# Kernel tuning notes

Measured on AMD Instinct MI355X. Metric: run time of the kernel, lower is better.

## Reference

```python
import jax, jax.numpy as jnp
import numpy as np

MASK_PENALTY = 1e15  # matches the TF module's additive mask constant


def setup_inputs() -> dict:
    key = jax.random.key(0)
    k1, k2, k3, k4, k5 = jax.random.split(key, 5)
    B, S, E, DK, DV = 4, 2048, 1024, 128, 128
    inputs = jax.random.normal(k1, (B, S, E), dtype=jnp.float32)
    mask = jax.random.randint(k2, (B, S, S), 0, 2, dtype=jnp.int32)
    # Dense kernels (glorot-ish scale)
    Wq = jax.random.normal(k3, (E, DK), dtype=jnp.float32) / np.float32(np.sqrt(E))
    Wk = jax.random.normal(k4, (E, DK), dtype=jnp.float32) / np.float32(np.sqrt(E))
    Wv = jax.random.normal(k5, (E, DV), dtype=jnp.float32) / np.float32(np.sqrt(E))
    return {"inputs": inputs, "mask": mask, "Wq": Wq, "Wk": Wk, "Wv": Wv}


def reference(inputs, mask, Wq, Wk, Wv):
    # q, k, v projections (no bias)
    q = jnp.einsum("bse,ed->bsd", inputs, Wq)  # [B,S,DK]
    k = jnp.einsum("bse,ed->bsd", inputs, Wk)  # [B,S,DK]
    v = jnp.einsum("bse,ed->bsd", inputs, Wv)  # [B,S,DV]
    dim_k = Wq.shape[-1]
    scale = jnp.asarray(1.0 / np.sqrt(dim_k), dtype=q.dtype)
    dot_p = jnp.einsum("bqd,bkd->bqk", q, k) * scale  # [B,S,S]
    dot_p = dot_p - MASK_PENALTY * mask.astype(dot_p.dtype)
    softm = jax.nn.softmax(dot_p, axis=-1)
    return jnp.einsum("bqk,bkd->bqd", softm, v)  # [B,S,DV]
```

## Files before the change

### kernel.cpp

```cpp
#include <hip/hip_runtime.h>
#include <stdint.h>


#define SEQ   2048
#define EDIM  1024
#define DDIM  128
#define QSCALE 0.08838834764831845f

typedef unsigned short u16;
using short8 = __attribute__((ext_vector_type(8))) short;
using f32x4  = __attribute__((ext_vector_type(4))) float;

__device__ __forceinline__ u16 f2bf(float x) {
    uint32_t u = __float_as_uint(x);
    return (u16)((u + 0x7fffu + ((u >> 16) & 1u)) >> 16);
}

__device__ __forceinline__ void gld16(const void* gsrc, void* lds_dst) {
    __builtin_amdgcn_global_load_lds(
        (const __attribute__((address_space(1))) uint32_t*)(uintptr_t)gsrc,
        (__attribute__((address_space(3))) uint32_t*)(uint32_t)(uintptr_t)lds_dst,
        16, 0, 0);
}

__global__ __launch_bounds__(256) void wprep_kernel(
    const float* __restrict__ Wq, const float* __restrict__ Wk, const float* __restrict__ Wv,
    u16* __restrict__ Wt)
{
    __shared__ u16 tl[64][65];
    const int t = blockIdx.x;
    const int wsel = t >> 5;
    const int tile = t & 31;
    const int k0 = (tile >> 1) * 64;
    const int n0 = (tile & 1) * 64;
    const float* W = (wsel == 0) ? Wq : ((wsel == 1) ? Wk : Wv);
#pragma unroll
    for (int it = 0; it < 16; ++it) {
        const int idx = it * 256 + threadIdx.x;
        const int r = idx >> 6, c = idx & 63;
        tl[c][r] = f2bf(W[(size_t)(k0 + r) * DDIM + n0 + c]);
    }
    __syncthreads();
    u16* Wtp = Wt + (size_t)wsel * DDIM * EDIM;
#pragma unroll
    for (int it = 0; it < 16; ++it) {
        const int idx = it * 256 + threadIdx.x;
        const int r = idx >> 6, c = idx & 63;
        Wtp[(size_t)(n0 + r) * EDIM + k0 + c] = tl[r][c];
    }
}

__global__ __launch_bounds__(256, 2) void proj_kernel(
    const float* __restrict__ Ain, const u16* __restrict__ Wtb,
    u16* __restrict__ Qb, u16* __restrict__ Kb, u16* __restrict__ Vtb)
{
    __shared__ __align__(16) uint8_t smem[24576];
    const int tid = threadIdx.x;
    const int w = tid >> 6, lane = tid & 63;
    const int lq = lane & 15, lg = lane >> 4;
    const int m0 = blockIdx.x * 64;
    const int wm = blockIdx.y;
    const u16* Wt = Wtb + (size_t)wm * DDIM * EDIM;

    f32x4 acc[8] = {};

#pragma unroll 1
    for (int kt = 0; kt < 16; ++kt) {
        const int k0 = kt * 64;
#pragma unroll
        for (int i = 0; i < 4; ++i) {
            const int G = i * 256 + tid;
            const int n = G >> 3, c = G & 7;
            gld16(Wt + (size_t)n * EDIM + k0 + (size_t)((c ^ (n & 7)) * 8),
                  smem + 8192 + i * 4096 + w * 1024);
        }
#pragma unroll
        for (int i = 0; i < 2; ++i) {
            const int G = i * 256 + tid;
            const int row = G >> 3, c = G & 7;
            const float* s2 = Ain + (size_t)(m0 + row) * EDIM + k0 + (c ^ (row & 7)) * 8;
            const f32x4 a0 = *(const f32x4*)s2;
            const f32x4 a1 = *(const f32x4*)(s2 + 4);
            short8 v;
            v[0] = (short)f2bf(a0[0]); v[1] = (short)f2bf(a0[1]);
            v[2] = (short)f2bf(a0[2]); v[3] = (short)f2bf(a0[3]);
            v[4] = (short)f2bf(a1[0]); v[5] = (short)f2bf(a1[1]);
            v[6] = (short)f2bf(a1[2]); v[7] = (short)f2bf(a1[3]);
            *(short8*)(smem + row * 128 + (c << 4)) = v;
        }
        __syncthreads();
#pragma unroll
        for (int ks = 0; ks < 2; ++ks) {
            const int arow = w * 16 + lq;
            const short8 af = *(const short8*)(smem + arow * 128 + ((((ks << 2) + lg) ^ (arow & 7)) << 4));
#pragma unroll
            for (int nf = 0; nf < 8; ++nf) {
                const int nrow = nf * 16 + lq;
                const short8 bfv = *(const short8*)(smem + 8192 + nrow * 128 + ((((ks << 2) + lg) ^ (nrow & 7)) << 4));
                acc[nf] = __builtin_amdgcn_mfma_f32_16x16x32_bf16(af, bfv, acc[nf], 0, 0, 0);
            }
        }
        __syncthreads();
    }

    if (wm < 2) {
        u16* Ot = (u16*)smem;
#pragma unroll
        for (int nf = 0; nf < 8; ++nf)
#pragma unroll
            for (int r = 0; r < 4; ++r)
                Ot[(size_t)(w * 16 + lg * 4 + r) * 128 + nf * 16 + lq] = f2bf(acc[nf][r]);
        __syncthreads();
        u16* dst = (wm == 0 ? Qb : Kb) + (size_t)m0 * 128;
#pragma unroll
        for (int i = 0; i < 4; ++i) {
            const int idx = (i * 256 + tid) * 8;
            *(short8*)(dst + idx) = *(const short8*)((const u16*)smem + idx);
        }
    } else {
#pragma unroll
        for (int nf = 0; nf < 8; ++nf)
#pragma unroll
            for (int r = 0; r < 4; ++r) {
                const int srow = w * 16 + lg * 4 + r;
                const int dcol = nf * 16 + lq;
                *(u16*)(smem + dcol * 128 + (((srow >> 3) ^ (dcol & 7)) << 4) + (srow & 7) * 2) = f2bf(acc[nf][r]);
            }
        __syncthreads();
        const int b = m0 >> 11;
        const int s0b = m0 & 2047;
        u16* dst = Vtb + (size_t)b * DDIM * SEQ;
#pragma unroll
        for (int i = 0; i < 4; ++i) {
            const int idx = i * 256 + tid;
            const int dd = idx >> 3, c = idx & 7;
            const short8 v2 = *(const short8*)(smem + dd * 128 + ((c ^ (dd & 7)) << 4));
            *(short8*)(dst + (size_t)dd * SEQ + s0b + c * 8) = v2;
        }
    }
}

__global__ __launch_bounds__(256, 2) void flash_kernel(
    const int* __restrict__ mask,
    const u16* __restrict__ Qb, const u16* __restrict__ Kb, const u16* __restrict__ Vtb,
    float* __restrict__ out)
{
    __shared__ __align__(16) uint8_t smem[69632];
    __shared__ float ml_m[4][16], ml_l[4][16], recipL[16];

    const int tid = threadIdx.x;
    const int w = tid >> 6, lane = tid & 63;
    const int lq = lane & 15, lg = lane >> 4;

    const int qt = blockIdx.x;
    const int b = qt >> 7;
    const int q0 = (qt & 127) << 4;
    const size_t qrow0 = (size_t)b * SEQ + q0;

    const u16* Qp = Qb + qrow0 * 128;
    const u16* Kp = Kb + (size_t)b * SEQ * 128;
    const u16* Vp = Vtb + (size_t)b * DDIM * SEQ;
    const int* mp = mask + ((size_t)b * SEQ + q0) * SEQ;

    short8 qf[4];
#pragma unroll
    for (int ks = 0; ks < 4; ++ks)
        qf[ks] = *(const short8*)(Qp + (size_t)lq * 128 + ks * 32 + lg * 8);

    f32x4 acc[8] = {};
    float mrow[4], lrow[4];
#pragma unroll
    for (int r = 0; r < 4; ++r) { mrow[r] = -1e30f; lrow[r] = 0.0f; }

    uint8_t* kvbase = smem + w * 16384;

#pragma unroll 1
    for (int t = 0; t < 16; ++t) {
        const int kv0 = w * 512 + t * 32;
        asm volatile("s_waitcnt lgkmcnt(0)" ::: "memory");
#pragma unroll
        for (int i = 0; i < 8; ++i) {
            const int G = i * 64 + lane;
            const int row = G >> 4, c = G & 15;
            gld16(Kp + (size_t)(kv0 + row) * 128 + (c ^ (row & 7)) * 8,
                  kvbase + i * 1024);
        }
#pragma unroll
        for (int i = 0; i < 8; ++i) {
            const int G = i * 64 + lane;
            const int dd = G >> 2, c = G & 3;
            gld16(Vp + (size_t)dd * SEQ + kv0 + (c ^ ((dd ^ (dd >> 2)) & 3)) * 8,
                  kvbase + 8192 + i * 1024);
        }
        int mv[2][4];
#pragma unroll
        for (int nf = 0; nf < 2; ++nf)
#pragma unroll
            for (int r = 0; r < 4; ++r)
                mv[nf][r] = mp[(size_t)(lg * 4 + r) * SEQ + kv0 + nf * 16 + lq];

        asm volatile("s_waitcnt vmcnt(0)" ::: "memory");

        f32x4 sacc[2] = {};
#pragma unroll
        for (int ks = 0; ks < 4; ++ks) {
#pragma unroll
            for (int nf = 0; nf < 2; ++nf) {
                const int krow = nf * 16 + lq;
                const short8 kf = *(const short8*)(kvbase + krow * 256 + ((((ks << 2) + lg) ^ (krow & 7)) << 4));
                sacc[nf] = __builtin_amdgcn_mfma_f32_16x16x32_bf16(qf[ks], kf, sacc[nf], 0, 0, 0);
            }
        }

        float sv[2][4], tm[4];
#pragma unroll
        for (int nf = 0; nf < 2; ++nf)
#pragma unroll
            for (int r = 0; r < 4; ++r)
                sv[nf][r] = sacc[nf][r] * QSCALE - 1e15f * (float)mv[nf][r];
#pragma unroll
        for (int r = 0; r < 4; ++r) tm[r] = fmaxf(sv[0][r], sv[1][r]);
#pragma unroll
        for (int d = 1; d < 16; d <<= 1)
#pragma unroll
            for (int r = 0; r < 4; ++r)
                tm[r] = fmaxf(tm[r], __shfl_xor(tm[r], d));

        float sf[4];
#pragma unroll
        for (int r = 0; r < 4; ++r) {
            const float mnew = fmaxf(mrow[r], tm[r]);
            sf[r] = __expf(mrow[r] - mnew);
            mrow[r] = mnew;
        }
        float p[2][4], rs[4];
#pragma unroll
        for (int nf = 0; nf < 2; ++nf)
#pragma unroll
            for (int r = 0; r < 4; ++r)
                p[nf][r] = __expf(sv[nf][r] - mrow[r]);
#pragma unroll
        for (int r = 0; r < 4; ++r) rs[r] = p[0][r] + p[1][r];
#pragma unroll
        for (int d = 1; d < 16; d <<= 1)
#pragma unroll
            for (int r = 0; r < 4; ++r)
                rs[r] += __shfl_xor(rs[r], d);
#pragma unroll
        for (int r = 0; r < 4; ++r) lrow[r] = lrow[r] * sf[r] + rs[r];
#pragma unroll
        for (int df = 0; df < 8; ++df)
#pragma unroll
            for (int r = 0; r < 4; ++r)
                acc[df][r] *= sf[r];

        uint8_t* pbase = smem + 65536 + w * 1024;
#pragma unroll
        for (int nf = 0; nf < 2; ++nf)
#pragma unroll
            for (int r = 0; r < 4; ++r) {
                const int row = lg * 4 + r, col = nf * 16 + lq;
                *(u16*)(pbase + row * 64 + ((((col >> 3) ^ ((row ^ (row >> 2)) & 3))) << 4) + (col & 7) * 2)
                    = f2bf(p[nf][r]);
            }
        const short8 pf = *(const short8*)(pbase + lq * 64 + ((lg ^ ((lq ^ (lq >> 2)) & 3)) << 4));
#pragma unroll
        for (int nf = 0; nf < 8; ++nf) {
            const int dd = nf * 16 + lq;
            const short8 vf = *(const short8*)(kvbase + 8192 + dd * 64 + ((lg ^ ((dd ^ (dd >> 2)) & 3)) << 4));
            acc[nf] = __builtin_amdgcn_mfma_f32_16x16x32_bf16(pf, vf, acc[nf], 0, 0, 0);
        }
    }

    if (lq == 0) {
#pragma unroll
        for (int r = 0; r < 4; ++r) {
            ml_m[w][lg * 4 + r] = mrow[r];
            ml_l[w][lg * 4 + r] = lrow[r];
        }
    }
    __syncthreads();
    float Lg[4];
#pragma unroll
    for (int r = 0; r < 4; ++r) {
        const int row = lg * 4 + r;
        const float m0v = ml_m[0][row], m1v = ml_m[1][row], m2v = ml_m[2][row], m3v = ml_m[3][row];
        const float mm = fmaxf(fmaxf(m0v, m1v), fmaxf(m2v, m3v));
        Lg[r] = ml_l[0][row] * __expf(m0v - mm) + ml_l[1][row] * __expf(m1v - mm)
              + ml_l[2][row] * __expf(m2v - mm) + ml_l[3][row] * __expf(m3v - mm);
        const float s = __expf(mrow[r] - mm);
#pragma unroll
        for (int df = 0; df < 8; ++df) acc[df][r] *= s;
    }
    if (w == 0 && lq == 0) {
#pragma unroll
        for (int r = 0; r < 4; ++r) recipL[lg * 4 + r] = 1.0f / Lg[r];
    }
    float* Ol = (float*)smem;
#pragma unroll
    for (int df = 0; df < 8; ++df)
#pragma unroll
        for (int r = 0; r < 4; ++r)
            Ol[(size_t)(w * 16 + lg * 4 + r) * 128 + df * 16 + lq] = acc[df][r];
    __syncthreads();

    {
        const int idx = tid * 8;
        const int row = idx >> 7, c0 = idx & 127;
        const float rl = recipL[row];
        f32x4 s0 = {}, s1 = {};
#pragma unroll
        for (int wv = 0; wv < 4; ++wv) {
            const float* p2 = Ol + (size_t)(wv * 16 + row) * 128 + c0;
            s0 += *(const f32x4*)p2;
            s1 += *(const f32x4*)(p2 + 4);
        }
        s0 *= rl; s1 *= rl;
        float* op = out + (qrow0 + row) * 128 + c0;
        *(f32x4*)op = s0;
        *(f32x4*)(op + 4) = s1;
    }
}

extern "C" void kernel_launch(void* const* d_in, const int* in_sizes, int n_in,
                              void* d_out, int out_size, void* d_ws, size_t ws_size,
                              hipStream_t stream) {
    (void)in_sizes; (void)n_in; (void)out_size; (void)ws_size;
    const float* inputs = (const float*)d_in[0];
    const int*   mask   = (const int*)d_in[1];
    const float* Wq     = (const float*)d_in[2];
    const float* Wk     = (const float*)d_in[3];
    const float* Wv     = (const float*)d_in[4];
    float* out = (float*)d_out;

    uint8_t* ws = (uint8_t*)d_ws;
    u16* Wtb = (u16*)ws;
    u16* Qb  = (u16*)(ws + 786432);
    u16* Kb  = (u16*)(ws + 2883584);
    u16* Vtb = (u16*)(ws + 4980736);

    hipLaunchKernelGGL(wprep_kernel, dim3(96), dim3(256), 0, stream, Wq, Wk, Wv, Wtb);
    hipLaunchKernelGGL(proj_kernel, dim3(128, 3), dim3(256), 0, stream, inputs, Wtb, Qb, Kb, Vtb);
    hipLaunchKernelGGL(flash_kernel, dim3(512), dim3(256), 0, stream, mask, Qb, Kb, Vtb, out);
}
```

Before: 184.4 us.

## Bit-pack mask in prep pass, retile projection GEMM, fold Q scale, split waits

The int32 mask is packed into 32-bit bitmasks by a combined prep kernel, so the attention kernel reads 1 bit per mask element instead of 4 bytes. The projection GEMM moves to 128x128 tiles with a 2x2 wave layout and an XCD-aware block remap. The softmax scale is folded into Q at projection time. The flash kernel now waits only on K loads before QK^T and defers the V wait until the PV step. The flash blocks are also remapped across XCDs. The mask is still read in full once in prep, and the bigger projection tiles cut the grid to 192 blocks, which lowers parallelism.

Measured after the change: 188.4 us. 2.2% more time.

```diff
diff --git a/kernel.cpp b/kernel.cpp
--- a/kernel.cpp
+++ b/kernel.cpp
@@ -8,8 +8,10 @@
 #define QSCALE 0.08838834764831845f
 
 typedef unsigned short u16;
+typedef unsigned int   u32;
 using short8 = __attribute__((ext_vector_type(8))) short;
 using f32x4  = __attribute__((ext_vector_type(4))) float;
+using int4v  = __attribute__((ext_vector_type(4))) int;
 
 __device__ __forceinline__ u16 f2bf(float x) {
     uint32_t u = __float_as_uint(x);
@@ -23,30 +25,47 @@
         16, 0, 0);
 }
 
-__global__ __launch_bounds__(256) void wprep_kernel(
+__global__ __launch_bounds__(256) void prep_kernel(
+    const int* __restrict__ mask,
     const float* __restrict__ Wq, const float* __restrict__ Wk, const float* __restrict__ Wv,
-    u16* __restrict__ Wt)
+    u32* __restrict__ Mbits, u16* __restrict__ Wt)
 {
     __shared__ u16 tl[64][65];
-    const int t = blockIdx.x;
-    const int wsel = t >> 5;
-    const int tile = t & 31;
-    const int k0 = (tile >> 1) * 64;
-    const int n0 = (tile & 1) * 64;
-    const float* W = (wsel == 0) ? Wq : ((wsel == 1) ? Wk : Wv);
-#pragma unroll
-    for (int it = 0; it < 16; ++it) {
-        const int idx = it * 256 + threadIdx.x;
-        const int r = idx >> 6, c = idx & 63;
-        tl[c][r] = f2bf(W[(size_t)(k0 + r) * DDIM + n0 + c]);
-    }
-    __syncthreads();
-    u16* Wtp = Wt + (size_t)wsel * DDIM * EDIM;
-#pragma unroll
-    for (int it = 0; it < 16; ++it) {
-        const int idx = it * 256 + threadIdx.x;
-        const int r = idx >> 6, c = idx & 63;
-        Wtp[(size_t)(n0 + r) * EDIM + k0 + c] = tl[r][c];
+    const int bx = blockIdx.x;
+    if (bx < 2048) {
+        const int word = bx * 256 + threadIdx.x;
+        const int* src = mask + (size_t)word * 32;
+        u32 bits = 0;
+#pragma unroll
+        for (int it = 0; it < 8; ++it) {
+            const int4v v = *(const int4v*)(src + it * 4);
+            bits |= (v[0] != 0 ? 1u : 0u) << (it * 4 + 0);
+            bits |= (v[1] != 0 ? 1u : 0u) << (it * 4 + 1);
+            bits |= (v[2] != 0 ? 1u : 0u) << (it * 4 + 2);
+            bits |= (v[3] != 0 ? 1u : 0u) << (it * 4 + 3);
+        }
+        Mbits[word] = bits;
+    } else {
+        const int t = bx - 2048;
+        const int wsel = t >> 5;
+        const int tile = t & 31;
+        const int k0 = (tile >> 1) * 64;
+        const int n0 = (tile & 1) * 64;
+        const float* W = (wsel == 0) ? Wq : ((wsel == 1) ? Wk : Wv);
+#pragma unroll
+        for (int it = 0; it < 16; ++it) {
+            const int idx = it * 256 + threadIdx.x;
+            const int r = idx >> 6, c = idx & 63;
+            tl[c][r] = f2bf(W[(size_t)(k0 + r) * DDIM + n0 + c]);
+        }
+        __syncthreads();
+        u16* Wtp = Wt + (size_t)wsel * DDIM * EDIM;
+#pragma unroll
+        for (int it = 0; it < 16; ++it) {
+            const int idx = it * 256 + threadIdx.x;
+            const int r = idx >> 6, c = idx & 63;
+            Wtp[(size_t)(n0 + r) * EDIM + k0 + c] = tl[r][c];
+        }
     }
 }
 
@@ -54,15 +73,19 @@
     const float* __restrict__ Ain, const u16* __restrict__ Wtb,
     u16* __restrict__ Qb, u16* __restrict__ Kb, u16* __restrict__ Vtb)
 {
-    __shared__ __align__(16) uint8_t smem[24576];
+    __shared__ __align__(16) uint8_t smem[32768];
     const int tid = threadIdx.x;
     const int w = tid >> 6, lane = tid & 63;
     const int lq = lane & 15, lg = lane >> 4;
-    const int m0 = blockIdx.x * 64;
-    const int wm = blockIdx.y;
+    const int wr = w >> 1, wc = w & 1;
+
+    const int bid = blockIdx.x;
+    const int wg = (bid & 7) * 24 + (bid >> 3);
+    const int wm = wg % 3;
+    const int m0 = (wg / 3) * 128;
     const u16* Wt = Wtb + (size_t)wm * DDIM * EDIM;
 
-    f32x4 acc[8] = {};
+    f32x4 acc[4][4] = {};
 
 #pragma unroll 1
     for (int kt = 0; kt < 16; ++kt) {
@@ -71,14 +94,14 @@
         for (int i = 0; i < 4; ++i) {
             const int G = i * 256 + tid;
             const int n = G >> 3, c = G & 7;
-            gld16(Wt + (size_t)n * EDIM + k0 + (size_t)((c ^ (n & 7)) * 8),
-                  smem + 8192 + i * 4096 + w * 1024);
-        }
-#pragma unroll
-        for (int i = 0; i < 2; ++i) {
+            gld16(Wt + (size_t)n * EDIM + k0 + ((c ^ (n & 7)) << 3),
+                  smem + 16384 + i * 4096 + w * 1024);
+        }
+#pragma unroll
+        for (int i = 0; i < 4; ++i) {
             const int G = i * 256 + tid;
             const int row = G >> 3, c = G & 7;
-            const float* s2 = Ain + (size_t)(m0 + row) * EDIM + k0 + (c ^ (row & 7)) * 8;
+            const float* s2 = Ain + (size_t)(m0 + row) * EDIM + k0 + ((c ^ (row & 7)) << 3);
             const f32x4 a0 = *(const f32x4*)s2;
             const f32x4 a1 = *(const f32x4*)(s2 + 4);
             short8 v;
@@ -91,57 +114,75 @@
         __syncthreads();
 #pragma unroll
         for (int ks = 0; ks < 2; ++ks) {
-            const int arow = w * 16 + lq;
-            const short8 af = *(const short8*)(smem + arow * 128 + ((((ks << 2) + lg) ^ (arow & 7)) << 4));
-#pragma unroll
-            for (int nf = 0; nf < 8; ++nf) {
-                const int nrow = nf * 16 + lq;
-                const short8 bfv = *(const short8*)(smem + 8192 + nrow * 128 + ((((ks << 2) + lg) ^ (nrow & 7)) << 4));
-                acc[nf] = __builtin_amdgcn_mfma_f32_16x16x32_bf16(af, bfv, acc[nf], 0, 0, 0);
+            short8 af[4], bfv[4];
+#pragma unroll
+            for (int mf = 0; mf < 4; ++mf) {
+                const int arow = wr * 64 + mf * 16 + lq;
+                af[mf] = *(const short8*)(smem + arow * 128 + ((((ks << 2) + lg) ^ (arow & 7)) << 4));
             }
-        }
-        __syncthreads();
-    }
-
+#pragma unroll
+            for (int nf = 0; nf < 4; ++nf) {
+                const int brow = wc * 64 + nf * 16 + lq;
+                bfv[nf] = *(const short8*)(smem + 16384 + brow * 128 + ((((ks << 2) + lg) ^ (brow & 7)) << 4));
+            }
+#pragma unroll
+            for (int mf = 0; mf < 4; ++mf)
+#pragma unroll
+                for (int nf = 0; nf < 4; ++nf)
+                    acc[mf][nf] = __builtin_amdgcn_mfma_f32_16x16x32_bf16(af[mf], bfv[nf], acc[mf][nf], 0, 0, 0);
+        }
+        __syncthreads();
+    }
+
+    const float osc = (wm == 0) ? QSCALE : 1.0f;
     if (wm < 2) {
-        u16* Ot = (u16*)smem;
-#pragma unroll
-        for (int nf = 0; nf < 8; ++nf)
-#pragma unroll
-            for (int r = 0; r < 4; ++r)
-                Ot[(size_t)(w * 16 + lg * 4 + r) * 128 + nf * 16 + lq] = f2bf(acc[nf][r]);
+#pragma unroll
+        for (int mf = 0; mf < 4; ++mf)
+#pragma unroll
+            for (int nf = 0; nf < 4; ++nf)
+#pragma unroll
+                for (int rr = 0; rr < 4; ++rr) {
+                    const int row = wr * 64 + mf * 16 + lg * 4 + rr;
+                    const int col = wc * 64 + nf * 16 + lq;
+                    *(u16*)(smem + row * 256 + (((col >> 3) ^ (row & 7)) << 4) + ((col & 7) << 1))
+                        = f2bf(acc[mf][nf][rr] * osc);
+                }
         __syncthreads();
         u16* dst = (wm == 0 ? Qb : Kb) + (size_t)m0 * 128;
 #pragma unroll
-        for (int i = 0; i < 4; ++i) {
-            const int idx = (i * 256 + tid) * 8;
-            *(short8*)(dst + idx) = *(const short8*)((const u16*)smem + idx);
+        for (int i = 0; i < 8; ++i) {
+            const int j = i * 256 + tid;
+            const int row = j >> 4, c = j & 15;
+            *(short8*)(dst + (size_t)row * 128 + c * 8)
+                = *(const short8*)(smem + row * 256 + ((c ^ (row & 7)) << 4));
         }
     } else {
 #pragma unroll
-        for (int nf = 0; nf < 8; ++nf)
-#pragma unroll
-            for (int r = 0; r < 4; ++r) {
-                const int srow = w * 16 + lg * 4 + r;
-                const int dcol = nf * 16 + lq;
-                *(u16*)(smem + dcol * 128 + (((srow >> 3) ^ (dcol & 7)) << 4) + (srow & 7) * 2) = f2bf(acc[nf][r]);
-            }
-        __syncthreads();
-        const int b = m0 >> 11;
-        const int s0b = m0 & 2047;
+        for (int mf = 0; mf < 4; ++mf)
+#pragma unroll
+            for (int nf = 0; nf < 4; ++nf)
+#pragma unroll
+                for (int rr = 0; rr < 4; ++rr) {
+                    const int sl = wr * 64 + mf * 16 + lg * 4 + rr;
+                    const int d  = wc * 64 + nf * 16 + lq;
+                    *(u16*)(smem + d * 256 + (((sl >> 3) ^ (d & 7)) << 4) + ((sl & 7) << 1))
+                        = f2bf(acc[mf][nf][rr]);
+                }
+        __syncthreads();
+        const int b = m0 >> 11, s0b = m0 & 2047;
         u16* dst = Vtb + (size_t)b * DDIM * SEQ;
 #pragma unroll
-        for (int i = 0; i < 4; ++i) {
-            const int idx = i * 256 + tid;
-            const int dd = idx >> 3, c = idx & 7;
-            const short8 v2 = *(const short8*)(smem + dd * 128 + ((c ^ (dd & 7)) << 4));
-            *(short8*)(dst + (size_t)dd * SEQ + s0b + c * 8) = v2;
+        for (int i = 0; i < 8; ++i) {
+            const int j = i * 256 + tid;
+            const int dd = j >> 4, c = j & 15;
+            *(short8*)(dst + (size_t)dd * SEQ + s0b + c * 8)
+                = *(const short8*)(smem + dd * 256 + ((c ^ (dd & 7)) << 4));
         }
     }
 }
 
 __global__ __launch_bounds__(256, 2) void flash_kernel(
-    const int* __restrict__ mask,
+    const u32* __restrict__ Mb,
     const u16* __restrict__ Qb, const u16* __restrict__ Kb, const u16* __restrict__ Vtb,
     float* __restrict__ out)
 {
@@ -152,7 +193,8 @@
     const int w = tid >> 6, lane = tid & 63;
     const int lq = lane & 15, lg = lane >> 4;
 
-    const int qt = blockIdx.x;
+    const int bid = blockIdx.x;
+    const int qt = (bid & 7) * 64 + (bid >> 3);
     const int b = qt >> 7;
     const int q0 = (qt & 127) << 4;
     const size_t qrow0 = (size_t)b * SEQ + q0;
@@ -160,7 +202,6 @@
     const u16* Qp = Qb + qrow0 * 128;
     const u16* Kp = Kb + (size_t)b * SEQ * 128;
     const u16* Vp = Vtb + (size_t)b * DDIM * SEQ;
-    const int* mp = mask + ((size_t)b * SEQ + q0) * SEQ;
 
     short8 qf[4];
 #pragma unroll
@@ -177,7 +218,9 @@
 #pragma unroll 1
     for (int t = 0; t < 16; ++t) {
         const int kv0 = w * 512 + t * 32;
+        const int kvw = w * 16 + t;
         asm volatile("s_waitcnt lgkmcnt(0)" ::: "memory");
+        __builtin_amdgcn_sched_barrier(0);
 #pragma unroll
         for (int i = 0; i < 8; ++i) {
             const int G = i * 64 + lane;
@@ -185,6 +228,12 @@
             gld16(Kp + (size_t)(kv0 + row) * 128 + (c ^ (row & 7)) * 8,
                   kvbase + i * 1024);
         }
+        __builtin_amdgcn_sched_barrier(0);
+        u32 mw[4];
+#pragma unroll
+        for (int r = 0; r < 4; ++r)
+            mw[r] = Mb[(qrow0 + lg * 4 + r) * 64 + kvw];
+        __builtin_amdgcn_sched_barrier(0);
 #pragma unroll
         for (int i = 0; i < 8; ++i) {
             const int G = i * 64 + lane;
@@ -192,14 +241,8 @@
             gld16(Vp + (size_t)dd * SEQ + kv0 + (c ^ ((dd ^ (dd >> 2)) & 3)) * 8,
                   kvbase + 8192 + i * 1024);
         }
-        int mv[2][4];
-#pragma unroll
-        for (int nf = 0; nf < 2; ++nf)
-#pragma unroll
-            for (int r = 0; r < 4; ++r)
-                mv[nf][r] = mp[(size_t)(lg * 4 + r) * SEQ + kv0 + nf * 16 + lq];
-
-        asm volatile("s_waitcnt vmcnt(0)" ::: "memory");
+        __builtin_amdgcn_sched_barrier(0);
+        asm volatile("s_waitcnt vmcnt(8)" ::: "memory");
 
         f32x4 sacc[2] = {};
 #pragma unroll
@@ -214,10 +257,10 @@
 
         float sv[2][4], tm[4];
 #pragma unroll
-        for (int nf = 0; nf < 2; ++nf)
-#pragma unroll
-            for (int r = 0; r < 4; ++r)
-                sv[nf][r] = sacc[nf][r] * QSCALE - 1e15f * (float)mv[nf][r];
+        for (int r = 0; r < 4; ++r) {
+            sv[0][r] = sacc[0][r] + (((mw[r] >> lq) & 1u)        ? -1e15f : 0.0f);
+            sv[1][r] = sacc[1][r] + (((mw[r] >> (16 + lq)) & 1u) ? -1e15f : 0.0f);
+        }
 #pragma unroll
         for (int r = 0; r < 4; ++r) tm[r] = fmaxf(sv[0][r], sv[1][r]);
 #pragma unroll
@@ -264,6 +307,8 @@
                     = f2bf(p[nf][r]);
             }
         const short8 pf = *(const short8*)(pbase + lq * 64 + ((lg ^ ((lq ^ (lq >> 2)) & 3)) << 4));
+        asm volatile("s_waitcnt vmcnt(0)" ::: "memory");
+        __builtin_amdgcn_sched_barrier(0);
 #pragma unroll
         for (int nf = 0; nf < 8; ++nf) {
             const int dd = nf * 16 + lq;
@@ -334,12 +379,13 @@
     float* out = (float*)d_out;
 
     uint8_t* ws = (uint8_t*)d_ws;
-    u16* Wtb = (u16*)ws;
-    u16* Qb  = (u16*)(ws + 786432);
-    u16* Kb  = (u16*)(ws + 2883584);
-    u16* Vtb = (u16*)(ws + 4980736);
-
-    hipLaunchKernelGGL(wprep_kernel, dim3(96), dim3(256), 0, stream, Wq, Wk, Wv, Wtb);
-    hipLaunchKernelGGL(proj_kernel, dim3(128, 3), dim3(256), 0, stream, inputs, Wtb, Qb, Kb, Vtb);
-    hipLaunchKernelGGL(flash_kernel, dim3(512), dim3(256), 0, stream, mask, Qb, Kb, Vtb, out);
-}
+    u16* Wtb   = (u16*)ws;
+    u16* Qb    = (u16*)(ws + 786432);
+    u16* Kb    = (u16*)(ws + 2883584);
+    u16* Vtb   = (u16*)(ws + 4980736);
+    u32* Mbits = (u32*)(ws + 7077888);
+
+    hipLaunchKernelGGL(prep_kernel, dim3(2144), dim3(256), 0, stream, mask, Wq, Wk, Wv, Mbits, Wtb);
+    hipLaunchKernelGGL(proj_kernel, dim3(192), dim3(256), 0, stream, inputs, Wtb, Qb, Kb, Vtb);
+    hipLaunchKernelGGL(flash_kernel, dim3(512), dim3(256), 0, stream, Mbits, Qb, Kb, Vtb, out);
+}
```
